# Kernel tuning notes

Hardware: AMD Instinct MI355X
Metric: run time of the kernel (lower is better)

## Reference

```python
import jax, jax.numpy as jnp
import numpy as np

B, T, C, H, HS, L, V, BITS = 4, 512, 768, 12, 64, 12, 50257, 16


def _ln(x, g, b, eps=1e-5):
    m = x.mean(-1, keepdims=True)
    v = ((x - m) ** 2).mean(-1, keepdims=True)
    return (x - m) * jax.lax.rsqrt(v + eps) * g + b


def setup_inputs() -> dict:
    key = jax.random.key(0)
    ks = jax.random.split(key, 12)
    s = 0.02
    return {
        "idx": jax.random.randint(ks[0], (B, T), 0, V),
        "tok_emb": jax.random.normal(ks[1], (V, C), jnp.float32) * s,
        "pos_emb": jax.random.normal(ks[2], (T, C), jnp.float32) * s,
        "Wq": jax.random.normal(ks[3], (L, H, C, HS), jnp.float32) * s,
        "Wk": jax.random.normal(ks[4], (L, H, C, HS), jnp.float32) * s,
        "Wv": jax.random.normal(ks[5], (L, H, C, HS), jnp.float32) * s,
        "Wo": jax.random.normal(ks[6], (L, C, C), jnp.float32) * s,
        "bo": jnp.zeros((L, C), jnp.float32),
        "W1": jax.random.normal(ks[7], (L, C, 4 * C), jnp.float32) * s,
        "b1": jnp.zeros((L, 4 * C), jnp.float32),
        "W2": jax.random.normal(ks[8], (L, 4 * C, C), jnp.float32) * s,
        "b2": jnp.zeros((L, C), jnp.float32),
        "ln1_g": jnp.ones((L, C), jnp.float32),
        "ln1_b": jnp.zeros((L, C), jnp.float32),
        "ln2_g": jnp.ones((L, C), jnp.float32),
        "ln2_b": jnp.zeros((L, C), jnp.float32),
        "lnf_g": jnp.ones((C,), jnp.float32),
        "lnf_b": jnp.zeros((C,), jnp.float32),
        "Wh": jax.random.normal(ks[9], (C, BITS), jnp.float32) * s,
        "bh": jnp.zeros((BITS,), jnp.float32),
    }


def reference(idx, tok_emb, pos_emb, Wq, Wk, Wv, Wo, bo, W1, b1, W2, b2,
              ln1_g, ln1_b, ln2_g, ln2_b, lnf_g, lnf_b, Wh, bh):
    Bc, Tc = idx.shape
    x = tok_emb[idx] + pos_emb[:Tc]          # [B,T,C]
    mask = jnp.tril(jnp.ones((Tc, Tc), bool))  # causal tril buffer
    scale = HS ** -0.5

    def block(x, p):
        wq, wk, wv, wo, bo_, w1, b1_, w2, b2_, g1, bb1, g2, bb2 = p
        xn = _ln(x, g1, bb1)
        q = jnp.einsum('btc,hcd->bhtd', xn, wq)
        k = jnp.einsum('btc,hcd->bhtd', xn, wk)
        v = jnp.einsum('btc,hcd->bhtd', xn, wv)
        wei = jnp.einsum('bhtd,bhsd->bhts', q, k) * scale
        wei = jnp.where(mask, wei, -jnp.inf)
        wei = jax.nn.softmax(wei, axis=-1)
        o = jnp.einsum('bhts,bhsd->bhtd', wei, v)
        o = o.transpose(0, 2, 1, 3).reshape(Bc, Tc, H * HS)  # concat heads
        x = x + o @ wo + bo_
        xn2 = _ln(x, g2, bb2)
        h = jax.nn.gelu(xn2 @ w1 + b1_, approximate=False)  # exact GELU (torch default)
        x = x + h @ w2 + b2_
        return x, None

    x, _ = jax.lax.scan(block, x, (Wq, Wk, Wv, Wo, bo, W1, b1, W2, b2,
                                   ln1_g, ln1_b, ln2_g, ln2_b))
    x = _ln(x, lnf_g, lnf_b)
    logits = x @ Wh + bh                      # [B,T,16] ECOC logits
    return logits
```

## Files before the change

### kernel.cpp

```cpp
#include <hip/hip_runtime.h>
#include <hip/hip_bf16.h>
#include <math.h>

#define TT   512
#define CC   768
#define HH   12
#define HSZ  64
#define LL   12
#define C4   3072
#define BTOT 2048
#define NQKV 2304
#define NX   ((long)BTOT * CC)

typedef __attribute__((ext_vector_type(8))) short short8;
typedef __attribute__((ext_vector_type(4))) float f32x4;

__device__ __forceinline__ unsigned short f2b_bits(float f) {
    unsigned u = __float_as_uint(f);
    return (unsigned short)((u + 0x7fffu + ((u >> 16) & 1u)) >> 16);
}
__device__ __forceinline__ float b2f(unsigned short b) {
    return __uint_as_float((unsigned)b << 16);
}

__device__ __forceinline__ void gl_lds16(const void* g, void* l) {
    __builtin_amdgcn_global_load_lds(
        (const __attribute__((address_space(1))) unsigned int*)g,
        (__attribute__((address_space(3))) unsigned int*)l,
        16, 0, 0);
}

__global__ __launch_bounds__(256) void embed_k(const int* __restrict__ idx,
    const float* __restrict__ tok, const float* __restrict__ pos,
    float* __restrict__ x)
{
    int r   = blockIdx.x;
    int tid = threadIdx.x;
    int t   = r & (TT - 1);
    long id = idx[r];
    const float* te = tok + id * (long)CC;
    const float* pe = pos + (long)t * CC;
    float* xr = x + (long)r * CC;
#pragma unroll
    for (int i = 0; i < 3; ++i) {
        int c = tid + i * 256;
        xr[c] = te[c] + pe[c];
    }
}

__global__ __launch_bounds__(256) void ln_b(const float* __restrict__ x,
    const float* __restrict__ g, const float* __restrict__ b,
    __hip_bfloat16* __restrict__ y)
{
    int r = blockIdx.x, tid = threadIdx.x;
    const float* xr = x + (long)r * CC;
    float v[3];
    v[0] = xr[tid]; v[1] = xr[tid + 256]; v[2] = xr[tid + 512];
    float s  = v[0] + v[1] + v[2];
    float sq = v[0]*v[0] + v[1]*v[1] + v[2]*v[2];
#pragma unroll
    for (int off = 32; off > 0; off >>= 1) {
        s  += __shfl_down(s, off);
        sq += __shfl_down(sq, off);
    }
    __shared__ float ss[4], ssq[4];
    int w = tid >> 6;
    if ((tid & 63) == 0) { ss[w] = s; ssq[w] = sq; }
    __syncthreads();
    s  = ss[0] + ss[1] + ss[2] + ss[3];
    sq = ssq[0] + ssq[1] + ssq[2] + ssq[3];
    float mean = s * (1.0f / CC);
    float var  = sq * (1.0f / CC) - mean * mean;
    float rs   = rsqrtf(var + 1e-5f);
    __hip_bfloat16* yr = y + (long)r * CC;
#pragma unroll
    for (int i = 0; i < 3; ++i) {
        int c = tid + i * 256;
        yr[c] = __float2bfloat16((v[i] - mean) * rs * g[c] + b[c]);
    }
}

template <bool DOLN>
__global__ __launch_bounds__(256) void red_ln(float* __restrict__ x,
    const unsigned short* __restrict__ p, const float* __restrict__ bias,
    const float* __restrict__ g, const float* __restrict__ b,
    __hip_bfloat16* __restrict__ y)
{
    int r = blockIdx.x, tid = threadIdx.x;
    float* xr = x + (long)r * CC;
    const unsigned short* pr = p + (long)r * CC;
    float v[3];
#pragma unroll
    for (int i = 0; i < 3; ++i) {
        int c = tid + i * 256;
        float s = xr[c] + bias[c];
        s += b2f(pr[c]);
        s += b2f(pr[c + 1 * NX]);
        s += b2f(pr[c + 2 * NX]);
        s += b2f(pr[c + 3 * NX]);
        xr[c] = s;
        v[i] = s;
    }
    if (!DOLN) return;
    float s  = v[0] + v[1] + v[2];
    float sq = v[0]*v[0] + v[1]*v[1] + v[2]*v[2];
#pragma unroll
    for (int off = 32; off > 0; off >>= 1) {
        s  += __shfl_down(s, off);
        sq += __shfl_down(sq, off);
    }
    __shared__ float ss[4], ssq[4];
    int w = tid >> 6;
    if ((tid & 63) == 0) { ss[w] = s; ssq[w] = sq; }
    __syncthreads();
    s  = ss[0] + ss[1] + ss[2] + ss[3];
    sq = ssq[0] + ssq[1] + ssq[2] + ssq[3];
    float mean = s * (1.0f / CC);
    float var  = sq * (1.0f / CC) - mean * mean;
    float rs   = rsqrtf(var + 1e-5f);
    __hip_bfloat16* yr = y + (long)r * CC;
#pragma unroll
    for (int i = 0; i < 3; ++i) {
        int c = tid + i * 256;
        yr[c] = __float2bfloat16((v[i] - mean) * rs * g[c] + b[c]);
    }
}

__global__ __launch_bounds__(256) void cvtT_k(const float* __restrict__ src,
    __hip_bfloat16* __restrict__ dst, int R, int D, long sSrc, long sDst)
{
    src += (long)blockIdx.z * sSrc;
    dst += (long)blockIdx.z * sDst;
    __shared__ float t[64][65];
    int d0 = blockIdx.x * 64, r0 = blockIdx.y * 64;
    int tid = threadIdx.x;
#pragma unroll
    for (int i = 0; i < 4; ++i) {
        int flat = tid + i * 256;
        int r = flat >> 4, c4 = (flat & 15) * 4;
        float4 v = *(const float4*)&src[(long)(r0 + r) * D + d0 + c4];
        t[r][c4 + 0] = v.x; t[r][c4 + 1] = v.y;
        t[r][c4 + 2] = v.z; t[r][c4 + 3] = v.w;
    }
    __syncthreads();
#pragma unroll
    for (int i = 0; i < 4; ++i) {
        int flat = tid + i * 256;
        int n = flat >> 4, kq = (flat & 15) * 4;
        ushort4 o;
        o.x = f2b_bits(t[kq + 0][n]); o.y = f2b_bits(t[kq + 1][n]);
        o.z = f2b_bits(t[kq + 2][n]); o.w = f2b_bits(t[kq + 3][n]);
        *(ushort4*)&dst[(long)(d0 + n) * R + r0 + kq] = o;
    }
}

__global__ __launch_bounds__(256) void cvt_qkvT(const float* __restrict__ Wq,
    const float* __restrict__ Wk, const float* __restrict__ Wv,
    __hip_bfloat16* __restrict__ out)
{
    int c0 = blockIdx.x * 64;
    int g  = blockIdx.y;
    int l  = blockIdx.z;
    int which = g / 12, h = g % 12;
    const long wAtt = (long)HH * CC * HSZ;
    const float* src = (which == 0 ? Wq : which == 1 ? Wk : Wv)
                       + l * wAtt + (long)h * CC * HSZ;
    __hip_bfloat16* dst = out + (long)l * NQKV * CC + (long)(which * CC + h * HSZ) * CC;
    __shared__ float t[64][65];
    int tid = threadIdx.x;
#pragma unroll
    for (int i = 0; i < 4; ++i) {
        int flat = tid + i * 256;
        int r = flat >> 4, c4 = (flat & 15) * 4;
        float4 v = *(const float4*)&src[(long)(c0 + r) * HSZ + c4];
        t[r][c4 + 0] = v.x; t[r][c4 + 1] = v.y;
        t[r][c4 + 2] = v.z; t[r][c4 + 3] = v.w;
    }
    __syncthreads();
#pragma unroll
    for (int i = 0; i < 4; ++i) {
        int flat = tid + i * 256;
        int n = flat >> 4, kq = (flat & 15) * 4;
        ushort4 o;
        o.x = f2b_bits(t[kq + 0][n]); o.y = f2b_bits(t[kq + 1][n]);
        o.z = f2b_bits(t[kq + 2][n]); o.w = f2b_bits(t[kq + 3][n]);
        *(ushort4*)&dst[(long)n * CC + c0 + kq] = o;
    }
}

template <int EPI>
__global__ __launch_bounds__(256, 3) void gemm_bf16(
    const __hip_bfloat16* __restrict__ A,
    const __hip_bfloat16* __restrict__ BT,
    __hip_bfloat16* __restrict__ Cb, float* __restrict__ Cf,
    const float* __restrict__ bias, __hip_bfloat16* __restrict__ Vt,
    int K, int lda, int ldb, int ldc)
{
    __shared__ short Asm[4][64 * 32];
    __shared__ short Bsm[4][128 * 32];
    const int tid  = threadIdx.x;
    const int lane = tid & 63;
    const int wid  = tid >> 6;
    const int wm = wid >> 1, wn = wid & 1;

    const int gx = gridDim.x;
    const int slice = gx * gridDim.y;
    int flat = blockIdx.y * gx + blockIdx.x;
    int swz  = (flat & 7) * (slice >> 3) + (flat >> 3);
    const int row0 = (swz / gx) * 64, col0 = (swz % gx) * 128;
    const int sk = (EPI == 5) ? blockIdx.z : 0;

    const int gr = tid >> 2;
    const int cb = ((tid & 3) + (tid >> 3)) & 3;
    const int gk = cb * 8;
    const __hip_bfloat16* Ap = A  + (long)(row0 + gr) * lda + sk * K + gk;
    const __hip_bfloat16* Bp = BT + (long)(col0 + gr) * ldb + sk * K + gk;
    const int lofs = wid * 512;

    f32x4 acc[2][4] = {};
    const int fr = lane & 15, g = lane >> 4;

    int offA[2], offB[4];
#pragma unroll
    for (int m = 0; m < 2; ++m) {
        int row = wm * 32 + m * 16 + fr;
        offA[m] = row * 32 + (((g - (row >> 1)) & 3) * 8);
    }
#pragma unroll
    for (int n = 0; n < 4; ++n) {
        int row = wn * 64 + n * 16 + fr;
        offB[n] = row * 32 + (((g - (row >> 1)) & 3) * 8);
    }

#define STAGE(buf)                                                          \
    do {                                                                    \
        gl_lds16(Ap, &Asm[buf][lofs]);                                      \
        gl_lds16(Bp, &Bsm[buf][lofs]);                                      \
        gl_lds16(Bp + (long)64 * ldb, &Bsm[buf][lofs + 64 * 32]);           \
        Ap += 32; Bp += 32;                                                 \
    } while (0)

    STAGE(0); STAGE(1); STAGE(2);

    const int nt = K >> 5;
    for (int t = 0; t < nt; ++t) {
        if (t < nt - 2)       asm volatile("s_waitcnt vmcnt(6)" ::: "memory");
        else if (t == nt - 2) asm volatile("s_waitcnt vmcnt(3)" ::: "memory");
        else                  asm volatile("s_waitcnt vmcnt(0)" ::: "memory");
        __builtin_amdgcn_s_barrier();
        __builtin_amdgcn_sched_barrier(0);
        if (t + 3 < nt) STAGE((t + 3) & 3);

        const int cur = t & 3;
        short8 af[2], bf[4];
#pragma unroll
        for (int m = 0; m < 2; ++m)
            af[m] = *(const short8*)&Asm[cur][offA[m]];
#pragma unroll
        for (int n = 0; n < 4; ++n)
            bf[n] = *(const short8*)&Bsm[cur][offB[n]];
#pragma unroll
        for (int m = 0; m < 2; ++m)
#pragma unroll
            for (int n = 0; n < 4; ++n)
                acc[m][n] = __builtin_amdgcn_mfma_f32_16x16x32_bf16(
                    af[m], bf[n], acc[m][n], 0, 0, 0);
    }
#undef STAGE

    const int fq = lane >> 4;
#pragma unroll
    for (int m = 0; m < 2; ++m) {
        int rbase = row0 + wm * 32 + m * 16 + fq * 4;
#pragma unroll
        for (int n = 0; n < 4; ++n) {
            int col = col0 + wn * 64 + n * 16 + fr;
            if (EPI == 1 && col >= 1536) {
                int hd = col - 1536;
                int b = rbase >> 9, t = rbase & (TT - 1);
                ushort4 o;
                o.x = f2b_bits(acc[m][n][0]); o.y = f2b_bits(acc[m][n][1]);
                o.z = f2b_bits(acc[m][n][2]); o.w = f2b_bits(acc[m][n][3]);
                *(ushort4*)&Vt[((long)(b * HH + (hd >> 6)) * HSZ + (hd & 63)) * TT + t] = o;
                continue;
            }
            float bv = (EPI == 2) ? bias[col] : 0.f;
#pragma unroll
            for (int j = 0; j < 4; ++j) {
                long row = rbase + j;
                float v = acc[m][n][j];
                if (EPI == 1) {
                    Cb[row * ldc + col] = __float2bfloat16(v);
                } else if (EPI == 2) {
                    v += bv;
                    v = 0.5f * v * (1.0f + erff(v * 0.70710678118654752f));
                    Cb[row * ldc + col] = __float2bfloat16(v);
                } else {
                    Cb[(long)sk * NX + row * ldc + col] = __float2bfloat16(v);
                }
            }
        }
    }
}

__global__ __launch_bounds__(64) void attn_mfma(
    const __hip_bfloat16* __restrict__ qkv,
    const __hip_bfloat16* __restrict__ vT,
    __hip_bfloat16* __restrict__ o)
{
    int flat = blockIdx.x + 32 * (blockIdx.y + 12 * blockIdx.z);
    int swz  = (flat & 7) * 192 + (flat >> 3);
    const int qt = swz & 31;
    const int h  = (swz >> 5) % 12;
    const int b  = swz / 384;
    const int lane = threadIdx.x;
    const int t0 = qt * 16;
    const int fr = lane & 15, g = lane >> 4;

    __shared__ unsigned short P_lds[16 * 40];
    __shared__ float corr_lds[16], l_lds[16];

    const long qbase = ((long)(b * TT + t0 + fr)) * NQKV + h * HSZ + g * 8;
    short8 qf0 = *(const short8*)(qkv + qbase);
    short8 qf1 = *(const short8*)(qkv + qbase + 32);

    f32x4 oacc[4] = {};
    float m_run = -3.0e38f, l_run = 0.f;
    const int t_lane = t0 + fr;
    const int smax = t0 + 15;
    const long kcol = CC + h * HSZ + g * 8;
    const long vrow = (((long)(b * HH + h) * HSZ) + fr) * TT + g * 8;

    short8 ka0, ka1, ka2, ka3;
    {
        long kb0 = ((long)(b * TT + fr)) * NQKV + kcol;
        long kb1 = ((long)(b * TT + 16 + fr)) * NQKV + kcol;
        ka0 = *(const short8*)(qkv + kb0);
        ka1 = *(const short8*)(qkv + kb0 + 32);
        ka2 = *(const short8*)(qkv + kb1);
        ka3 = *(const short8*)(qkv + kb1 + 32);
    }

    for (int s0 = 0; s0 <= smax; s0 += 32) {
        f32x4 st0 = {}, st1 = {};
        st0 = __builtin_amdgcn_mfma_f32_16x16x32_bf16(ka0, qf0, st0, 0, 0, 0);
        st0 = __builtin_amdgcn_mfma_f32_16x16x32_bf16(ka1, qf1, st0, 0, 0, 0);
        st1 = __builtin_amdgcn_mfma_f32_16x16x32_bf16(ka2, qf0, st1, 0, 0, 0);
        st1 = __builtin_amdgcn_mfma_f32_16x16x32_bf16(ka3, qf1, st1, 0, 0, 0);

        const bool more = (s0 + 32 <= smax);
        short8 kn0, kn1, kn2, kn3;
        if (more) {
            long kb0 = ((long)(b * TT + s0 + 32 + fr)) * NQKV + kcol;
            long kb1 = ((long)(b * TT + s0 + 48 + fr)) * NQKV + kcol;
            kn0 = *(const short8*)(qkv + kb0);
            kn1 = *(const short8*)(qkv + kb0 + 32);
            kn2 = *(const short8*)(qkv + kb1);
            kn3 = *(const short8*)(qkv + kb1 + 32);
        }
        short8 vc0 = *(const short8*)(vT + vrow + s0);
        short8 vc1 = *(const short8*)(vT + vrow + 16 * TT + s0);
        short8 vc2 = *(const short8*)(vT + vrow + 32 * TT + s0);
        short8 vc3 = *(const short8*)(vT + vrow + 48 * TT + s0);

        float p[8];
        float mx = -3.0e38f;
#pragma unroll
        for (int j = 0; j < 4; ++j) {
            int s = s0 + g * 4 + j;
            float v = st0[j] * 0.125f;
            v = (s <= t_lane) ? v : -3.0e38f;
            p[j] = v; mx = fmaxf(mx, v);
        }
#pragma unroll
        for (int j = 0; j < 4; ++j) {
            int s = s0 + 16 + g * 4 + j;
            float v = st1[j] * 0.125f;
            v = (s <= t_lane) ? v : -3.0e38f;
            p[4 + j] = v; mx = fmaxf(mx, v);
        }
        mx = fmaxf(mx, __shfl_xor(mx, 16));
        mx = fmaxf(mx, __shfl_xor(mx, 32));
        float mnew = fmaxf(m_run, mx);
        float corr = __expf(m_run - mnew);
        float psum = 0.f;
#pragma unroll
        for (int i = 0; i < 8; ++i) {
            float e = __expf(p[i] - mnew);
            p[i] = e; psum += e;
        }
        psum += __shfl_xor(psum, 16);
        psum += __shfl_xor(psum, 32);
        l_run = l_run * corr + psum;
        m_run = mnew;

        if (lane < 16) corr_lds[lane] = corr;
        unsigned u0 = (unsigned)f2b_bits(p[0]) | ((unsigned)f2b_bits(p[1]) << 16);
        unsigned u1 = (unsigned)f2b_bits(p[2]) | ((unsigned)f2b_bits(p[3]) << 16);
        unsigned u2 = (unsigned)f2b_bits(p[4]) | ((unsigned)f2b_bits(p[5]) << 16);
        unsigned u3 = (unsigned)f2b_bits(p[6]) | ((unsigned)f2b_bits(p[7]) << 16);
        *(unsigned*)&P_lds[fr * 40 + g * 4]          = u0;
        *(unsigned*)&P_lds[fr * 40 + g * 4 + 2]      = u1;
        *(unsigned*)&P_lds[fr * 40 + 16 + g * 4]     = u2;
        *(unsigned*)&P_lds[fr * 40 + 16 + g * 4 + 2] = u3;
        __builtin_amdgcn_sched_barrier(0);

        float cr0 = corr_lds[g * 4 + 0], cr1 = corr_lds[g * 4 + 1];
        float cr2 = corr_lds[g * 4 + 2], cr3 = corr_lds[g * 4 + 3];
        short8 pf = *(const short8*)&P_lds[fr * 40 + g * 8];
        oacc[0][0] *= cr0; oacc[0][1] *= cr1; oacc[0][2] *= cr2; oacc[0][3] *= cr3;
        oacc[0] = __builtin_amdgcn_mfma_f32_16x16x32_bf16(pf, vc0, oacc[0], 0, 0, 0);
        oacc[1][0] *= cr0; oacc[1][1] *= cr1; oacc[1][2] *= cr2; oacc[1][3] *= cr3;
        oacc[1] = __builtin_amdgcn_mfma_f32_16x16x32_bf16(pf, vc1, oacc[1], 0, 0, 0);
        oacc[2][0] *= cr0; oacc[2][1] *= cr1; oacc[2][2] *= cr2; oacc[2][3] *= cr3;
        oacc[2] = __builtin_amdgcn_mfma_f32_16x16x32_bf16(pf, vc2, oacc[2], 0, 0, 0);
        oacc[3][0] *= cr0; oacc[3][1] *= cr1; oacc[3][2] *= cr2; oacc[3][3] *= cr3;
        oacc[3] = __builtin_amdgcn_mfma_f32_16x16x32_bf16(pf, vc3, oacc[3], 0, 0, 0);

        if (more) { ka0 = kn0; ka1 = kn1; ka2 = kn2; ka3 = kn3; }
        __builtin_amdgcn_sched_barrier(0);
    }

    if (lane < 16) l_lds[lane] = l_run;
    __builtin_amdgcn_sched_barrier(0);
    float il0 = 1.f / l_lds[g * 4 + 0], il1 = 1.f / l_lds[g * 4 + 1];
    float il2 = 1.f / l_lds[g * 4 + 2], il3 = 1.f / l_lds[g * 4 + 3];
#pragma unroll
    for (int dt = 0; dt < 4; ++dt) {
        long cbase = (long)(b * TT + t0) * CC + h * HSZ + dt * 16 + fr;
        o[cbase + (g * 4 + 0) * (long)CC] = __float2bfloat16(oacc[dt][0] * il0);
        o[cbase + (g * 4 + 1) * (long)CC] = __float2bfloat16(oacc[dt][1] * il1);
        o[cbase + (g * 4 + 2) * (long)CC] = __float2bfloat16(oacc[dt][2] * il2);
        o[cbase + (g * 4 + 3) * (long)CC] = __float2bfloat16(oacc[dt][3] * il3);
    }
}

__global__ __launch_bounds__(256) void head_k(const float* __restrict__ x,
    const float* __restrict__ g, const float* __restrict__ bb,
    const float* __restrict__ Wh, const float* __restrict__ bh,
    float* __restrict__ out)
{
    int r = blockIdx.x, tid = threadIdx.x;
    const float* xr = x + (long)r * CC;
    float v[3];
    v[0] = xr[tid]; v[1] = xr[tid + 256]; v[2] = xr[tid + 512];
    float s  = v[0] + v[1] + v[2];
    float sq = v[0]*v[0] + v[1]*v[1] + v[2]*v[2];
#pragma unroll
    for (int off = 32; off > 0; off >>= 1) {
        s  += __shfl_down(s, off);
        sq += __shfl_down(sq, off);
    }
    __shared__ float ss[4], ssq[4];
    int w = tid >> 6;
    if ((tid & 63) == 0) { ss[w] = s; ssq[w] = sq; }
    __syncthreads();
    s  = ss[0] + ss[1] + ss[2] + ss[3];
    sq = ssq[0] + ssq[1] + ssq[2] + ssq[3];
    float mean = s * (1.0f / CC);
    float var  = sq * (1.0f / CC) - mean * mean;
    float rs   = rsqrtf(var + 1e-5f);

    float acc[16];
#pragma unroll
    for (int j = 0; j < 16; ++j) acc[j] = 0.f;
#pragma unroll
    for (int i = 0; i < 3; ++i) {
        int c = tid + i * 256;
        float xnv = (v[i] - mean) * rs * g[c] + bb[c];
        const float* wr = Wh + (long)c * 16;
#pragma unroll
        for (int j = 0; j < 16; ++j) acc[j] = fmaf(xnv, wr[j], acc[j]);
    }
#pragma unroll
    for (int off = 32; off > 0; off >>= 1)
#pragma unroll
        for (int j = 0; j < 16; ++j) acc[j] += __shfl_down(acc[j], off);
    __shared__ float red[4][16];
    if ((tid & 63) == 0)
#pragma unroll
        for (int j = 0; j < 16; ++j) red[w][j] = acc[j];
    __syncthreads();
    if (tid < 16)
        out[(long)r * 16 + tid] =
            red[0][tid] + red[1][tid] + red[2][tid] + red[3][tid] + bh[tid];
}

extern "C" void kernel_launch(void* const* d_in, const int* in_sizes, int n_in,
                              void* d_out, int out_size, void* d_ws, size_t ws_size,
                              hipStream_t stream)
{
    const int*   idx  = (const int*)  d_in[0];
    const float* tok  = (const float*)d_in[1];
    const float* pos  = (const float*)d_in[2];
    const float* Wq   = (const float*)d_in[3];
    const float* Wk   = (const float*)d_in[4];
    const float* Wv   = (const float*)d_in[5];
    const float* Wo   = (const float*)d_in[6];
    const float* bo   = (const float*)d_in[7];
    const float* W1   = (const float*)d_in[8];
    const float* b1   = (const float*)d_in[9];
    const float* W2   = (const float*)d_in[10];
    const float* b2   = (const float*)d_in[11];
    const float* ln1g = (const float*)d_in[12];
    const float* ln1b = (const float*)d_in[13];
    const float* ln2g = (const float*)d_in[14];
    const float* ln2b = (const float*)d_in[15];
    const float* lnfg = (const float*)d_in[16];
    const float* lnfb = (const float*)d_in[17];
    const float* Wh   = (const float*)d_in[18];
    const float* bh   = (const float*)d_in[19];

    char* w = (char*)d_ws;
    float*          x     = (float*)w;          w += NX * 4;
    __hip_bfloat16* xn_b  = (__hip_bfloat16*)w; w += NX * 2;
    __hip_bfloat16* qkvb  = (__hip_bfloat16*)w; w += (long)BTOT * NQKV * 2;
    __hip_bfloat16* vT    = (__hip_bfloat16*)w; w += NX * 2;
    __hip_bfloat16* o_b   = (__hip_bfloat16*)w; w += NX * 2;
    __hip_bfloat16* hb    = (__hip_bfloat16*)w; w += (long)BTOT * C4 * 2;
    __hip_bfloat16* qkvT  = (__hip_bfloat16*)w; w += (long)LL * NQKV * CC * 2;
    __hip_bfloat16* woT   = (__hip_bfloat16*)w; w += (long)LL * CC * CC * 2;
    __hip_bfloat16* w1T   = (__hip_bfloat16*)w; w += (long)LL * C4 * CC * 2;
    __hip_bfloat16* w2T   = (__hip_bfloat16*)w; w += (long)LL * CC * C4 * 2;
    __hip_bfloat16* pbuf  = (__hip_bfloat16*)w; w += 4 * NX * 2;

    cvt_qkvT<<<dim3(12, 36, LL), 256, 0, stream>>>(Wq, Wk, Wv, qkvT);
    cvtT_k<<<dim3(12, 12, LL), 256, 0, stream>>>(Wo, woT, CC, CC,
        (long)CC * CC, (long)CC * CC);
    cvtT_k<<<dim3(48, 12, LL), 256, 0, stream>>>(W1, w1T, CC, C4,
        (long)CC * C4, (long)CC * C4);
    cvtT_k<<<dim3(12, 48, LL), 256, 0, stream>>>(W2, w2T, C4, CC,
        (long)C4 * CC, (long)C4 * CC);

    embed_k<<<BTOT, 256, 0, stream>>>(idx, tok, pos, x);
    ln_b<<<BTOT, 256, 0, stream>>>(x, ln1g, ln1b, xn_b);

    for (int l = 0; l < LL; ++l) {
        gemm_bf16<1><<<dim3(NQKV / 128, BTOT / 64), 256, 0, stream>>>(
            xn_b, qkvT + (long)l * NQKV * CC, qkvb, nullptr, nullptr, vT,
            CC, CC, CC, NQKV);

        attn_mfma<<<dim3(TT / 16, HH, 4), 64, 0, stream>>>(qkvb, vT, o_b);

        gemm_bf16<5><<<dim3(CC / 128, BTOT / 64, 4), 256, 0, stream>>>(
            o_b, woT + (long)l * CC * CC, pbuf, nullptr, nullptr, nullptr,
            192, CC, CC, CC);

        red_ln<true><<<BTOT, 256, 0, stream>>>(x, (const unsigned short*)pbuf,
            bo + l * CC, ln2g + l * CC, ln2b + l * CC, xn_b);

        gemm_bf16<2><<<dim3(C4 / 128, BTOT / 64), 256, 0, stream>>>(
            xn_b, w1T + (long)l * C4 * CC, hb, nullptr, b1 + l * C4, nullptr,
            CC, CC, CC, C4);

        gemm_bf16<5><<<dim3(CC / 128, BTOT / 64, 4), 256, 0, stream>>>(
            hb, w2T + (long)l * CC * C4, pbuf, nullptr, nullptr, nullptr,
            768, C4, C4, CC);

        if (l < LL - 1) {
            red_ln<true><<<BTOT, 256, 0, stream>>>(x, (const unsigned short*)pbuf,
                b2 + l * CC, ln1g + (l + 1) * CC, ln1b + (l + 1) * CC, xn_b);
        } else {
            red_ln<false><<<BTOT, 256, 0, stream>>>(x, (const unsigned short*)pbuf,
                b2 + l * CC, nullptr, nullptr, nullptr);
        }
    }

    head_k<<<BTOT, 256, 0, stream>>>(x, lnfg, lnfb, Wh, bh, (float*)d_out);
}
```

Baseline: 1.447 ms.

## Process two 16-row query tiles per attention wave to reuse K/V loads

Each attention wavefront now handles 32 query rows as two 16-row subtiles that share the same K and V fragments, halving the number of blocks and the redundant K/V global reads. The block swizzle is changed to match the new grid size. The cost is higher register pressure from doubled accumulators. Causal imbalance also grows, and the upper subtile does wasted masked work on the diagonal chunk.

Result: faster. 1.382 ms (-4.5%).

```diff
diff --git a/kernel.cpp b/kernel.cpp
--- a/kernel.cpp
+++ b/kernel.cpp
@@ -308,26 +308,30 @@
     const __hip_bfloat16* __restrict__ vT,
     __hip_bfloat16* __restrict__ o)
 {
-    int flat = blockIdx.x + 32 * (blockIdx.y + 12 * blockIdx.z);
-    int swz  = (flat & 7) * 192 + (flat >> 3);
-    const int qt = swz & 31;
-    const int h  = (swz >> 5) % 12;
-    const int b  = swz / 384;
+    int flat = blockIdx.x + 16 * (blockIdx.y + 12 * blockIdx.z);
+    int swz  = (flat & 7) * 96 + (flat >> 3);
+    const int qt = swz & 15;
+    const int h  = (swz >> 4) % 12;
+    const int b  = swz / 192;
     const int lane = threadIdx.x;
-    const int t0 = qt * 16;
+    const int t0 = qt * 32;
     const int fr = lane & 15, g = lane >> 4;
 
-    __shared__ unsigned short P_lds[16 * 40];
-    __shared__ float corr_lds[16], l_lds[16];
-
-    const long qbase = ((long)(b * TT + t0 + fr)) * NQKV + h * HSZ + g * 8;
-    short8 qf0 = *(const short8*)(qkv + qbase);
-    short8 qf1 = *(const short8*)(qkv + qbase + 32);
-
-    f32x4 oacc[4] = {};
-    float m_run = -3.0e38f, l_run = 0.f;
-    const int t_lane = t0 + fr;
-    const int smax = t0 + 15;
+    __shared__ unsigned short P_lds[32 * 40];
+    __shared__ float corr_lds[32], l_lds[32];
+
+    const long qbaseA = ((long)(b * TT + t0 + fr)) * NQKV + h * HSZ + g * 8;
+    const long qbaseB = qbaseA + (long)16 * NQKV;
+    short8 qfA0 = *(const short8*)(qkv + qbaseA);
+    short8 qfA1 = *(const short8*)(qkv + qbaseA + 32);
+    short8 qfB0 = *(const short8*)(qkv + qbaseB);
+    short8 qfB1 = *(const short8*)(qkv + qbaseB + 32);
+
+    f32x4 oaccA[4] = {}, oaccB[4] = {};
+    float mA = -3.0e38f, lA = 0.f, mB = -3.0e38f, lB = 0.f;
+    const int t_laneA = t0 + fr;
+    const int t_laneB = t0 + 16 + fr;
+    const int smax = t0 + 31;
     const long kcol = CC + h * HSZ + g * 8;
     const long vrow = (((long)(b * HH + h) * HSZ) + fr) * TT + g * 8;
 
@@ -342,11 +346,15 @@
     }
 
     for (int s0 = 0; s0 <= smax; s0 += 32) {
-        f32x4 st0 = {}, st1 = {};
-        st0 = __builtin_amdgcn_mfma_f32_16x16x32_bf16(ka0, qf0, st0, 0, 0, 0);
-        st0 = __builtin_amdgcn_mfma_f32_16x16x32_bf16(ka1, qf1, st0, 0, 0, 0);
-        st1 = __builtin_amdgcn_mfma_f32_16x16x32_bf16(ka2, qf0, st1, 0, 0, 0);
-        st1 = __builtin_amdgcn_mfma_f32_16x16x32_bf16(ka3, qf1, st1, 0, 0, 0);
+        f32x4 stA0 = {}, stA1 = {}, stB0 = {}, stB1 = {};
+        stA0 = __builtin_amdgcn_mfma_f32_16x16x32_bf16(ka0, qfA0, stA0, 0, 0, 0);
+        stA0 = __builtin_amdgcn_mfma_f32_16x16x32_bf16(ka1, qfA1, stA0, 0, 0, 0);
+        stA1 = __builtin_amdgcn_mfma_f32_16x16x32_bf16(ka2, qfA0, stA1, 0, 0, 0);
+        stA1 = __builtin_amdgcn_mfma_f32_16x16x32_bf16(ka3, qfA1, stA1, 0, 0, 0);
+        stB0 = __builtin_amdgcn_mfma_f32_16x16x32_bf16(ka0, qfB0, stB0, 0, 0, 0);
+        stB0 = __builtin_amdgcn_mfma_f32_16x16x32_bf16(ka1, qfB1, stB0, 0, 0, 0);
+        stB1 = __builtin_amdgcn_mfma_f32_16x16x32_bf16(ka2, qfB0, stB1, 0, 0, 0);
+        stB1 = __builtin_amdgcn_mfma_f32_16x16x32_bf16(ka3, qfB1, stB1, 0, 0, 0);
 
         const bool more = (s0 + 32 <= smax);
         short8 kn0, kn1, kn2, kn3;
@@ -363,75 +371,130 @@
         short8 vc2 = *(const short8*)(vT + vrow + 32 * TT + s0);
         short8 vc3 = *(const short8*)(vT + vrow + 48 * TT + s0);
 
-        float p[8];
-        float mx = -3.0e38f;
+        float pA[8];
+        float mxA = -3.0e38f;
 #pragma unroll
         for (int j = 0; j < 4; ++j) {
             int s = s0 + g * 4 + j;
-            float v = st0[j] * 0.125f;
-            v = (s <= t_lane) ? v : -3.0e38f;
-            p[j] = v; mx = fmaxf(mx, v);
+            float v = stA0[j] * 0.125f;
+            v = (s <= t_laneA) ? v : -3.0e38f;
+            pA[j] = v; mxA = fmaxf(mxA, v);
         }
 #pragma unroll
         for (int j = 0; j < 4; ++j) {
             int s = s0 + 16 + g * 4 + j;
-            float v = st1[j] * 0.125f;
-            v = (s <= t_lane) ? v : -3.0e38f;
-            p[4 + j] = v; mx = fmaxf(mx, v);
-        }
-        mx = fmaxf(mx, __shfl_xor(mx, 16));
-        mx = fmaxf(mx, __shfl_xor(mx, 32));
-        float mnew = fmaxf(m_run, mx);
-        float corr = __expf(m_run - mnew);
-        float psum = 0.f;
+            float v = stA1[j] * 0.125f;
+            v = (s <= t_laneA) ? v : -3.0e38f;
+            pA[4 + j] = v; mxA = fmaxf(mxA, v);
+        }
+        mxA = fmaxf(mxA, __shfl_xor(mxA, 16));
+        mxA = fmaxf(mxA, __shfl_xor(mxA, 32));
+        float mnewA = fmaxf(mA, mxA);
+        float corrA = __expf(mA - mnewA);
+        float psA = 0.f;
 #pragma unroll
         for (int i = 0; i < 8; ++i) {
-            float e = __expf(p[i] - mnew);
-            p[i] = e; psum += e;
-        }
-        psum += __shfl_xor(psum, 16);
-        psum += __shfl_xor(psum, 32);
-        l_run = l_run * corr + psum;
-        m_run = mnew;
-
-        if (lane < 16) corr_lds[lane] = corr;
-        unsigned u0 = (unsigned)f2b_bits(p[0]) | ((unsigned)f2b_bits(p[1]) << 16);
-        unsigned u1 = (unsigned)f2b_bits(p[2]) | ((unsigned)f2b_bits(p[3]) << 16);
-        unsigned u2 = (unsigned)f2b_bits(p[4]) | ((unsigned)f2b_bits(p[5]) << 16);
-        unsigned u3 = (unsigned)f2b_bits(p[6]) | ((unsigned)f2b_bits(p[7]) << 16);
-        *(unsigned*)&P_lds[fr * 40 + g * 4]          = u0;
-        *(unsigned*)&P_lds[fr * 40 + g * 4 + 2]      = u1;
-        *(unsigned*)&P_lds[fr * 40 + 16 + g * 4]     = u2;
-        *(unsigned*)&P_lds[fr * 40 + 16 + g * 4 + 2] = u3;
+            float e = __expf(pA[i] - mnewA);
+            pA[i] = e; psA += e;
+        }
+        psA += __shfl_xor(psA, 16);
+        psA += __shfl_xor(psA, 32);
+        lA = lA * corrA + psA;
+        mA = mnewA;
+
+        float pB[8];
+        float mxB = -3.0e38f;
+#pragma unroll
+        for (int j = 0; j < 4; ++j) {
+            int s = s0 + g * 4 + j;
+            float v = stB0[j] * 0.125f;
+            v = (s <= t_laneB) ? v : -3.0e38f;
+            pB[j] = v; mxB = fmaxf(mxB, v);
+        }
+#pragma unroll
+        for (int j = 0; j < 4; ++j) {
+            int s = s0 + 16 + g * 4 + j;
+            float v = stB1[j] * 0.125f;
+            v = (s <= t_laneB) ? v : -3.0e38f;
+            pB[4 + j] = v; mxB = fmaxf(mxB, v);
+        }
+        mxB = fmaxf(mxB, __shfl_xor(mxB, 16));
+        mxB = fmaxf(mxB, __shfl_xor(mxB, 32));
+        float mnewB = fmaxf(mB, mxB);
+        float corrB = __expf(mB - mnewB);
+        float psB = 0.f;
+#pragma unroll
+        for (int i = 0; i < 8; ++i) {
+            float e = __expf(pB[i] - mnewB);
+            pB[i] = e; psB += e;
+        }
+        psB += __shfl_xor(psB, 16);
+        psB += __shfl_xor(psB, 32);
+        lB = lB * corrB + psB;
+        mB = mnewB;
+
+        if (lane < 16) { corr_lds[lane] = corrA; corr_lds[16 + lane] = corrB; }
+        {
+            unsigned u0 = (unsigned)f2b_bits(pA[0]) | ((unsigned)f2b_bits(pA[1]) << 16);
+            unsigned u1 = (unsigned)f2b_bits(pA[2]) | ((unsigned)f2b_bits(pA[3]) << 16);
+            unsigned u2 = (unsigned)f2b_bits(pA[4]) | ((unsigned)f2b_bits(pA[5]) << 16);
+            unsigned u3 = (unsigned)f2b_bits(pA[6]) | ((unsigned)f2b_bits(pA[7]) << 16);
+            *(unsigned*)&P_lds[fr * 40 + g * 4]          = u0;
+            *(unsigned*)&P_lds[fr * 40 + g * 4 + 2]      = u1;
+            *(unsigned*)&P_lds[fr * 40 + 16 + g * 4]     = u2;
+            *(unsigned*)&P_lds[fr * 40 + 16 + g * 4 + 2] = u3;
+        }
+        {
+            unsigned u0 = (unsigned)f2b_bits(pB[0]) | ((unsigned)f2b_bits(pB[1]) << 16);
+            unsigned u1 = (unsigned)f2b_bits(pB[2]) | ((unsigned)f2b_bits(pB[3]) << 16);
+            unsigned u2 = (unsigned)f2b_bits(pB[4]) | ((unsigned)f2b_bits(pB[5]) << 16);
+            unsigned u3 = (unsigned)f2b_bits(pB[6]) | ((unsigned)f2b_bits(pB[7]) << 16);
+            *(unsigned*)&P_lds[(16 + fr) * 40 + g * 4]          = u0;
+            *(unsigned*)&P_lds[(16 + fr) * 40 + g * 4 + 2]      = u1;
+            *(unsigned*)&P_lds[(16 + fr) * 40 + 16 + g * 4]     = u2;
+            *(unsigned*)&P_lds[(16 + fr) * 40 + 16 + g * 4 + 2] = u3;
+        }
         __builtin_amdgcn_sched_barrier(0);
 
-        float cr0 = corr_lds[g * 4 + 0], cr1 = corr_lds[g * 4 + 1];
-        float cr2 = corr_lds[g * 4 + 2], cr3 = corr_lds[g * 4 + 3];
-        short8 pf = *(const short8*)&P_lds[fr * 40 + g * 8];
-        oacc[0][0] *= cr0; oacc[0][1] *= cr1; oacc[0][2] *= cr2; oacc[0][3] *= cr3;
-        oacc[0] = __builtin_amdgcn_mfma_f32_16x16x32_bf16(pf, vc0, oacc[0], 0, 0, 0);
-        oacc[1][0] *= cr0; oacc[1][1] *= cr1; oacc[1][2] *= cr2; oacc[1][3] *= cr3;
-        oacc[1] = __builtin_amdgcn_mfma_f32_16x16x32_bf16(pf, vc1, oacc[1], 0, 0, 0);
-        oacc[2][0] *= cr0; oacc[2][1] *= cr1; oacc[2][2] *= cr2; oacc[2][3] *= cr3;
-        oacc[2] = __builtin_amdgcn_mfma_f32_16x16x32_bf16(pf, vc2, oacc[2], 0, 0, 0);
-        oacc[3][0] *= cr0; oacc[3][1] *= cr1; oacc[3][2] *= cr2; oacc[3][3] *= cr3;
-        oacc[3] = __builtin_amdgcn_mfma_f32_16x16x32_bf16(pf, vc3, oacc[3], 0, 0, 0);
+        float crA0 = corr_lds[g * 4 + 0], crA1 = corr_lds[g * 4 + 1];
+        float crA2 = corr_lds[g * 4 + 2], crA3 = corr_lds[g * 4 + 3];
+        float crB0 = corr_lds[16 + g * 4 + 0], crB1 = corr_lds[16 + g * 4 + 1];
+        float crB2 = corr_lds[16 + g * 4 + 2], crB3 = corr_lds[16 + g * 4 + 3];
+        short8 pfA = *(const short8*)&P_lds[fr * 40 + g * 8];
+        short8 pfB = *(const short8*)&P_lds[(16 + fr) * 40 + g * 8];
+#pragma unroll
+        for (int dt = 0; dt < 4; ++dt) {
+            short8 vc = (dt == 0) ? vc0 : (dt == 1) ? vc1 : (dt == 2) ? vc2 : vc3;
+            oaccA[dt][0] *= crA0; oaccA[dt][1] *= crA1;
+            oaccA[dt][2] *= crA2; oaccA[dt][3] *= crA3;
+            oaccA[dt] = __builtin_amdgcn_mfma_f32_16x16x32_bf16(pfA, vc, oaccA[dt], 0, 0, 0);
+            oaccB[dt][0] *= crB0; oaccB[dt][1] *= crB1;
+            oaccB[dt][2] *= crB2; oaccB[dt][3] *= crB3;
+            oaccB[dt] = __builtin_amdgcn_mfma_f32_16x16x32_bf16(pfB, vc, oaccB[dt], 0, 0, 0);
+        }
 
         if (more) { ka0 = kn0; ka1 = kn1; ka2 = kn2; ka3 = kn3; }
         __builtin_amdgcn_sched_barrier(0);
     }
 
-    if (lane < 16) l_lds[lane] = l_run;
+    if (lane < 16) { l_lds[lane] = lA; l_lds[16 + lane] = lB; }
     __builtin_amdgcn_sched_barrier(0);
-    float il0 = 1.f / l_lds[g * 4 + 0], il1 = 1.f / l_lds[g * 4 + 1];
-    float il2 = 1.f / l_lds[g * 4 + 2], il3 = 1.f / l_lds[g * 4 + 3];
+    float ilA0 = 1.f / l_lds[g * 4 + 0], ilA1 = 1.f / l_lds[g * 4 + 1];
+    float ilA2 = 1.f / l_lds[g * 4 + 2], ilA3 = 1.f / l_lds[g * 4 + 3];
+    float ilB0 = 1.f / l_lds[16 + g * 4 + 0], ilB1 = 1.f / l_lds[16 + g * 4 + 1];
+    float ilB2 = 1.f / l_lds[16 + g * 4 + 2], ilB3 = 1.f / l_lds[16 + g * 4 + 3];
 #pragma unroll
     for (int dt = 0; dt < 4; ++dt) {
-        long cbase = (long)(b * TT + t0) * CC + h * HSZ + dt * 16 + fr;
-        o[cbase + (g * 4 + 0) * (long)CC] = __float2bfloat16(oacc[dt][0] * il0);
-        o[cbase + (g * 4 + 1) * (long)CC] = __float2bfloat16(oacc[dt][1] * il1);
-        o[cbase + (g * 4 + 2) * (long)CC] = __float2bfloat16(oacc[dt][2] * il2);
-        o[cbase + (g * 4 + 3) * (long)CC] = __float2bfloat16(oacc[dt][3] * il3);
+        long cbaseA = (long)(b * TT + t0) * CC + h * HSZ + dt * 16 + fr;
+        long cbaseB = cbaseA + (long)16 * CC;
+        o[cbaseA + (g * 4 + 0) * (long)CC] = __float2bfloat16(oaccA[dt][0] * ilA0);
+        o[cbaseA + (g * 4 + 1) * (long)CC] = __float2bfloat16(oaccA[dt][1] * ilA1);
+        o[cbaseA + (g * 4 + 2) * (long)CC] = __float2bfloat16(oaccA[dt][2] * ilA2);
+        o[cbaseA + (g * 4 + 3) * (long)CC] = __float2bfloat16(oaccA[dt][3] * ilA3);
+        o[cbaseB + (g * 4 + 0) * (long)CC] = __float2bfloat16(oaccB[dt][0] * ilB0);
+        o[cbaseB + (g * 4 + 1) * (long)CC] = __float2bfloat16(oaccB[dt][1] * ilB1);
+        o[cbaseB + (g * 4 + 2) * (long)CC] = __float2bfloat16(oaccB[dt][2] * ilB2);
+        o[cbaseB + (g * 4 + 3) * (long)CC] = __float2bfloat16(oaccB[dt][3] * ilB3);
     }
 }
 
@@ -540,7 +603,7 @@
             xn_b, qkvT + (long)l * NQKV * CC, qkvb, nullptr, nullptr, vT,
             CC, CC, CC, NQKV);
 
-        attn_mfma<<<dim3(TT / 16, HH, 4), 64, 0, stream>>>(qkvb, vT, o_b);
+        attn_mfma<<<dim3(TT / 32, HH, 4), 64, 0, stream>>>(qkvb, vT, o_b);
 
         gemm_bf16<5><<<dim3(CC / 128, BTOT / 64, 4), 256, 0, stream>>>(
             o_b, woT + (long)l * CC * CC, pbuf, nullptr, nullptr, nullptr,
```
